# Kernel optimization log

Measured on AMD Instinct MI355X. Metric: run time of the kernel, lower is better.

The kernel has to match this reference:

```python
import jax, jax.numpy as jnp
import numpy as np

B, S, D, H = 4, 2048, 1024, 16
DK = D // H


def setup_inputs() -> dict:
    key = jax.random.key(0)
    ks = jax.random.split(key, 11)
    inp = {
        'query': jax.random.normal(ks[0], (B, S, D), jnp.float32),
        'key': jax.random.normal(ks[1], (B, S, D), jnp.float32),
        'value': jax.random.normal(ks[2], (B, S, D), jnp.float32),
        'mask': jnp.tril(jnp.ones((1, 1, S, S), dtype=bool)),  # causal
    }
    sc = 1.0 / np.sqrt(D)
    inp['w_q'] = jax.random.normal(ks[3], (D, D), jnp.float32) * sc
    inp['b_q'] = jnp.zeros((D,), jnp.float32)
    inp['w_k'] = jax.random.normal(ks[4], (D, D), jnp.float32) * sc
    inp['b_k'] = jnp.zeros((D,), jnp.float32)
    inp['w_v'] = jax.random.normal(ks[5], (D, D), jnp.float32) * sc
    inp['b_v'] = jnp.zeros((D,), jnp.float32)
    inp['w_o'] = jax.random.normal(ks[6], (D, D), jnp.float32) * sc
    inp['b_o'] = jnp.zeros((D,), jnp.float32)
    return inp


def _split_heads(x):
    # Faithful to source: view(B, S, d_k, H) then permute(0,3,1,2)
    b, s, _ = x.shape
    return x.reshape(b, s, DK, H).transpose(0, 3, 1, 2)  # (B, H, S, DK)


def _concat_heads(x):
    # permute(0,2,1,3) -> reshape(B, S, d_k*H)
    b, h, s, dk = x.shape
    return x.transpose(0, 2, 1, 3).reshape(b, s, dk * h)


def reference(query, key, value, mask, w_q, b_q, w_k, b_k, w_v, b_v, w_o, b_o):
    q = query @ w_q.T + b_q
    k = key @ w_k.T + b_k
    v = value @ w_v.T + b_v
    q, k, v = _split_heads(q), _split_heads(k), _split_heads(v)
    scale = 1.0 / jnp.sqrt(jnp.asarray(DK, q.dtype))
    scores = jnp.einsum('bhqd,bhkd->bhqk', q, k) * scale
    scores = jnp.where(mask, scores, -jnp.inf)
    attn = jax.nn.softmax(scores, axis=-1)  # dropout p=0 -> identity
    out = jnp.einsum('bhqk,bhkd->bhqd', attn, v)
    return _concat_heads(out) @ w_o.T + b_o
```

## Files before the change

kernel.cpp:

```cpp
#include <hip/hip_runtime.h>

#define BB 4
#define SS 2048
#define DD 1024
#define HH 16
#define DK 64
#define MM (BB * SS)

typedef __bf16 bf16x8 __attribute__((ext_vector_type(8)));
typedef float f32x4 __attribute__((ext_vector_type(4)));
typedef unsigned short us8 __attribute__((ext_vector_type(8)));
typedef unsigned short us4 __attribute__((ext_vector_type(4)));

#define MFMA_BF16(a, b, c) __builtin_amdgcn_mfma_f32_16x16x32_bf16((a), (b), (c), 0, 0, 0)

__device__ __forceinline__ unsigned short f2bf(float f) {
  return __builtin_bit_cast(unsigned short, (__bf16)f);
}

__device__ __forceinline__ bf16x8 ld_frag(const unsigned short* p) {
  return __builtin_bit_cast(bf16x8, *(const us8*)p);
}

__device__ __forceinline__ void gl_lds16(const unsigned short* g, unsigned short* l) {
  __builtin_amdgcn_global_load_lds((const __attribute__((address_space(1))) void*)g,
                                   (__attribute__((address_space(3))) void*)l, 16, 0, 0);
}

__global__ void cvt_weights(const float* __restrict__ w0, const float* __restrict__ w1,
                            const float* __restrict__ w2, const float* __restrict__ w3,
                            unsigned short* __restrict__ dst) {
  const float* src = (blockIdx.y == 0) ? w0 : (blockIdx.y == 1) ? w1 : (blockIdx.y == 2) ? w2 : w3;
  unsigned short* d = dst + (size_t)blockIdx.y * (DD * DD);
  int idx = (blockIdx.x * 256 + threadIdx.x) * 4;
  float4 v = *(const float4*)(src + idx);
  us4 o;
  o[0] = f2bf(v.x); o[1] = f2bf(v.y); o[2] = f2bf(v.z); o[3] = f2bf(v.w);
  *(us4*)(d + idx) = o;
}

__global__ void cvt_x(const float* __restrict__ src, unsigned short* __restrict__ dst) {
  int idx = (blockIdx.x * 256 + threadIdx.x) * 8;
  float4 v0 = *(const float4*)(src + idx);
  float4 v1 = *(const float4*)(src + idx + 4);
  us8 o;
  o[0] = f2bf(v0.x); o[1] = f2bf(v0.y); o[2] = f2bf(v0.z); o[3] = f2bf(v0.w);
  o[4] = f2bf(v1.x); o[5] = f2bf(v1.y); o[6] = f2bf(v1.z); o[7] = f2bf(v1.w);
  *(us8*)(dst + idx) = o;
}

template <bool VMODE>
__global__ __launch_bounds__(256, 4) void qkv_gemm(
    const unsigned short* __restrict__ xb, const unsigned short* __restrict__ w,
    const float* __restrict__ bias, unsigned short* __restrict__ outp) {
  const int m0 = blockIdx.x * 128;
  const int h0 = blockIdx.y * 2;

  __shared__ unsigned short smem[17408];
  unsigned short* sA = smem;
  unsigned short* sB = smem + 4096;

  const int tid = threadIdx.x;
  const int lane = tid & 63;
  const int wave = tid >> 6;
  const int wm = wave & 1, wn = wave >> 1;
  const int quad = lane >> 4, l16 = lane & 15;

  f32x4 acc[4][4];
#pragma unroll
  for (int i = 0; i < 4; i++)
#pragma unroll
    for (int j = 0; j < 4; j++) acc[i][j] = f32x4{0.f, 0.f, 0.f, 0.f};

  for (int k0 = 0; k0 < DD; k0 += 32) {
    __syncthreads();
#pragma unroll
    for (int i = 0; i < 2; i++) {
      int idx = tid + i * 256;
      gl_lds16(xb + (size_t)(m0 + (idx >> 2)) * DD + k0 + ((idx & 3) << 3), sA + idx * 8);
    }
#pragma unroll
    for (int i = 0; i < 2; i++) {
      int idx = tid + i * 256;
      int c = idx >> 2;
      int n = ((c & 63) << 4) + h0 + (c >> 6);
      gl_lds16(w + (size_t)n * DD + k0 + ((idx & 3) << 3), sB + idx * 8);
    }
    __syncthreads();
    bf16x8 af[4];
#pragma unroll
    for (int mi = 0; mi < 4; mi++)
      af[mi] = ld_frag(sA + (wm * 64 + mi * 16 + l16) * 32 + quad * 8);
#pragma unroll
    for (int ni = 0; ni < 4; ni++) {
      bf16x8 bfr = ld_frag(sB + (wn * 64 + ni * 16 + l16) * 32 + quad * 8);
#pragma unroll
      for (int mi = 0; mi < 4; mi++) acc[mi][ni] = MFMA_BF16(af[mi], bfr, acc[mi][ni]);
    }
  }

  if (!VMODE) {
#pragma unroll
    for (int mi = 0; mi < 4; mi++) {
#pragma unroll
      for (int ni = 0; ni < 4; ni++) {
        int c = wn * 64 + ni * 16 + l16;
        int h = h0 + (c >> 6), dk = c & 63;
        float bvv = bias[(dk << 4) + h];
        int mg0 = m0 + wm * 64 + mi * 16 + quad * 4;
#pragma unroll
        for (int r = 0; r < 4; r++) {
          int mg = mg0 + r;
          int bb = mg >> 11, s = mg & 2047;
          size_t dst = ((size_t)((bb << 4) + h) * SS + s) * DK + dk;
          outp[dst] = f2bf(acc[mi][ni][r] + bvv);
        }
      }
    }
  } else {
    __syncthreads();
#pragma unroll
    for (int mi = 0; mi < 4; mi++) {
#pragma unroll
      for (int ni = 0; ni < 4; ni++) {
        int c = wn * 64 + ni * 16 + l16;
        int h = h0 + (c >> 6), dk = c & 63;
        float bvv = bias[(dk << 4) + h];
        int ml0 = wm * 64 + mi * 16 + quad * 4;
#pragma unroll
        for (int r = 0; r < 4; r++)
          smem[c * 136 + ml0 + r] = f2bf(acc[mi][ni][r] + bvv);
      }
    }
    __syncthreads();
    int bb = m0 >> 11;
    int sbase = m0 & 2047;
#pragma unroll
    for (int i = 0; i < 8; i++) {
      int idx = tid + i * 256;
      int c = idx >> 4, mc = (idx & 15) << 3;
      int h = h0 + (c >> 6), dk = c & 63;
      size_t dst = ((size_t)((bb << 4) + h) * DK + dk) * SS + sbase + mc;
      *(us8*)(outp + dst) = *(const us8*)(smem + c * 136 + mc);
    }
  }
}

__global__ __launch_bounds__(256, 2) void attn(
    const unsigned short* __restrict__ qh, const unsigned short* __restrict__ kh,
    const unsigned short* __restrict__ vt, unsigned short* __restrict__ outc) {
  const int bx = blockIdx.x;
  const int bh = blockIdx.y;
  const int b = bh >> 4, h = bh & 15;
  const unsigned short* Qp = qh + (size_t)bh * SS * DK;
  const unsigned short* Kp = kh + (size_t)bh * SS * DK;
  const unsigned short* Vp = vt + (size_t)bh * DK * SS;

  __shared__ unsigned short sK[128 * 72];
  __shared__ unsigned short sV[64 * 136];
  __shared__ unsigned short sP[128 * 132];

  const int tid = threadIdx.x;
  const int lane = tid & 63;
  const int wave = tid >> 6;
  const int quad = lane >> 4, l16 = lane & 15;
  const int wq0 = wave * 32;

  const float sl = 0.125f * 1.44269504088896f;

  for (int pass = 0; pass < 2; pass++) {
    const int qt = pass ? (15 - bx) : bx;
    const int q0 = qt * 128;

    bf16x8 aq[2][2];
#pragma unroll
    for (int mi = 0; mi < 2; mi++)
#pragma unroll
      for (int kk = 0; kk < 2; kk++)
        aq[mi][kk] = ld_frag(Qp + (size_t)(q0 + wq0 + mi * 16 + l16) * DK + kk * 32 + quad * 8);

    f32x4 o_acc[2][4];
    float mrowL[2], lrowL[2];
#pragma unroll
    for (int mi = 0; mi < 2; mi++) {
#pragma unroll
      for (int ni = 0; ni < 4; ni++) o_acc[mi][ni] = f32x4{0.f, 0.f, 0.f, 0.f};
      mrowL[mi] = -1e30f;
      lrowL[mi] = 0.f;
    }

    auto do_tile = [&](int kt, bool diag) {
      const int k0 = kt * 128;
      __syncthreads();
#pragma unroll
      for (int i = 0; i < 4; i++) {
        int idx = tid + i * 256;
        int row = idx >> 3, c8 = (idx & 7) << 3;
        *(us8*)(sK + row * 72 + c8) = *(const us8*)(Kp + (size_t)(k0 + row) * DK + c8);
      }
#pragma unroll
      for (int i = 0; i < 4; i++) {
        int idx = tid + i * 256;
        int row = idx >> 4, cc = (idx & 15) << 3;
        *(us8*)(sV + row * 136 + cc) = *(const us8*)(Vp + (size_t)row * SS + k0 + cc);
      }
      __syncthreads();

      f32x4 sc[2][8];
#pragma unroll
      for (int mi = 0; mi < 2; mi++)
#pragma unroll
        for (int kti = 0; kti < 8; kti++) sc[mi][kti] = f32x4{0.f, 0.f, 0.f, 0.f};
#pragma unroll
      for (int kti = 0; kti < 8; kti++) {
#pragma unroll
        for (int kk = 0; kk < 2; kk++) {
          bf16x8 ak = ld_frag(sK + (kti * 16 + l16) * 72 + kk * 32 + quad * 8);
#pragma unroll
          for (int mi = 0; mi < 2; mi++) sc[mi][kti] = MFMA_BF16(ak, aq[mi][kk], sc[mi][kti]);
        }
      }

      if (diag) {
#pragma unroll
        for (int mi = 0; mi < 2; mi++) {
          int ql = wq0 + mi * 16 + l16;
#pragma unroll
          for (int kti = 0; kti < 8; kti++)
#pragma unroll
            for (int r = 0; r < 4; r++) {
              int kl = kti * 16 + quad * 4 + r;
              float v = sc[mi][kti][r] * sl;
              sc[mi][kti][r] = (kl > ql) ? -1e30f : v;
            }
        }
      } else {
#pragma unroll
        for (int mi = 0; mi < 2; mi++)
#pragma unroll
          for (int kti = 0; kti < 8; kti++)
#pragma unroll
            for (int r = 0; r < 4; r++) sc[mi][kti][r] *= sl;
      }

      float alphaL[2];
#pragma unroll
      for (int mi = 0; mi < 2; mi++) {
        f32x4 vm = sc[mi][0];
#pragma unroll
        for (int kti = 1; kti < 8; kti++)
#pragma unroll
          for (int r = 0; r < 4; r++) vm[r] = fmaxf(vm[r], sc[mi][kti][r]);
        float mx = fmaxf(fmaxf(vm[0], vm[1]), fmaxf(vm[2], vm[3]));
        mx = fmaxf(mx, __shfl_xor(mx, 16, 64));
        mx = fmaxf(mx, __shfl_xor(mx, 32, 64));
        float mnew = fmaxf(mrowL[mi], mx);
        alphaL[mi] = exp2f(mrowL[mi] - mnew);
        mrowL[mi] = mnew;
      }

#pragma unroll
      for (int mi = 0; mi < 2; mi++) {
        f32x4 vs = f32x4{0.f, 0.f, 0.f, 0.f};
#pragma unroll
        for (int kti = 0; kti < 8; kti++) {
          us4 pk;
#pragma unroll
          for (int r = 0; r < 4; r++) {
            float p = exp2f(sc[mi][kti][r] - mrowL[mi]);
            vs[r] += p;
            pk[r] = f2bf(p);
          }
          *(us4*)(sP + (wq0 + mi * 16 + l16) * 132 + kti * 16 + quad * 4) = pk;
        }
        float ls = (vs[0] + vs[1]) + (vs[2] + vs[3]);
        ls += __shfl_xor(ls, 16, 64);
        ls += __shfl_xor(ls, 32, 64);
        lrowL[mi] = lrowL[mi] * alphaL[mi] + ls;
      }

#pragma unroll
      for (int mi = 0; mi < 2; mi++)
#pragma unroll
        for (int r = 0; r < 4; r++) {
          float a = __shfl(alphaL[mi], quad * 4 + r, 64);
#pragma unroll
          for (int ni = 0; ni < 4; ni++) o_acc[mi][ni][r] *= a;
        }

#pragma unroll
      for (int kk = 0; kk < 4; kk++) {
        bf16x8 ap[2];
#pragma unroll
        for (int mi = 0; mi < 2; mi++) {
          const unsigned short* base = sP + (wq0 + mi * 16 + l16) * 132 + kk * 32 + quad * 8;
          us4 lo = *(const us4*)base;
          us4 hi = *(const us4*)(base + 4);
          ap[mi] = __builtin_bit_cast(bf16x8, __builtin_shufflevector(lo, hi, 0, 1, 2, 3, 4, 5, 6, 7));
        }
#pragma unroll
        for (int ni = 0; ni < 4; ni++) {
          bf16x8 bfr = ld_frag(sV + (ni * 16 + l16) * 136 + kk * 32 + quad * 8);
#pragma unroll
          for (int mi = 0; mi < 2; mi++) o_acc[mi][ni] = MFMA_BF16(ap[mi], bfr, o_acc[mi][ni]);
        }
      }
    };

    for (int kt = 0; kt < qt; kt++) do_tile(kt, false);
    do_tile(qt, true);

#pragma unroll
    for (int mi = 0; mi < 2; mi++) {
#pragma unroll
      for (int r = 0; r < 4; r++) {
        float lr = __shfl(lrowL[mi], quad * 4 + r, 64);
        float inv = 1.0f / lr;
        int qg = q0 + wq0 + mi * 16 + quad * 4 + r;
        size_t rowbase = ((size_t)(b * SS + qg)) * DD + h * DK;
#pragma unroll
        for (int ni = 0; ni < 4; ni++) {
          int dk = ni * 16 + l16;
          outc[rowbase + dk] = f2bf(o_acc[mi][ni][r] * inv);
        }
      }
    }
  }
}

__global__ __launch_bounds__(256, 4) void out_proj(
    const unsigned short* __restrict__ ac, const unsigned short* __restrict__ wo,
    const float* __restrict__ bias, float* __restrict__ out) {
  const int m0 = blockIdx.x * 128;
  const int n0 = blockIdx.y * 128;
  __shared__ unsigned short sA[128 * 32];
  __shared__ unsigned short sB[128 * 32];

  const int tid = threadIdx.x;
  const int lane = tid & 63;
  const int wave = tid >> 6;
  const int wm = wave & 1, wn = wave >> 1;
  const int quad = lane >> 4, l16 = lane & 15;

  f32x4 acc[4][4];
#pragma unroll
  for (int i = 0; i < 4; i++)
#pragma unroll
    for (int j = 0; j < 4; j++) acc[i][j] = f32x4{0.f, 0.f, 0.f, 0.f};

  for (int k0 = 0; k0 < DD; k0 += 32) {
    __syncthreads();
#pragma unroll
    for (int i = 0; i < 2; i++) {
      int idx = tid + i * 256;
      gl_lds16(ac + (size_t)(m0 + (idx >> 2)) * DD + k0 + ((idx & 3) << 3), sA + idx * 8);
    }
#pragma unroll
    for (int i = 0; i < 2; i++) {
      int idx = tid + i * 256;
      gl_lds16(wo + (size_t)(n0 + (idx >> 2)) * DD + k0 + ((idx & 3) << 3), sB + idx * 8);
    }
    __syncthreads();
    bf16x8 af[4];
#pragma unroll
    for (int mi = 0; mi < 4; mi++)
      af[mi] = ld_frag(sA + (wm * 64 + mi * 16 + l16) * 32 + quad * 8);
#pragma unroll
    for (int ni = 0; ni < 4; ni++) {
      bf16x8 bfr = ld_frag(sB + (wn * 64 + ni * 16 + l16) * 32 + quad * 8);
#pragma unroll
      for (int mi = 0; mi < 4; mi++) acc[mi][ni] = MFMA_BF16(af[mi], bfr, acc[mi][ni]);
    }
  }

#pragma unroll
  for (int mi = 0; mi < 4; mi++) {
#pragma unroll
    for (int ni = 0; ni < 4; ni++) {
      int n = n0 + wn * 64 + ni * 16 + l16;
      float bvv = bias[n];
      int mg0 = m0 + wm * 64 + mi * 16 + quad * 4;
#pragma unroll
      for (int r = 0; r < 4; r++) out[(size_t)(mg0 + r) * DD + n] = acc[mi][ni][r] + bvv;
    }
  }
}

extern "C" void kernel_launch(void* const* d_in, const int* in_sizes, int n_in,
                              void* d_out, int out_size, void* d_ws, size_t ws_size,
                              hipStream_t stream) {
  const float* q_in = (const float*)d_in[0];
  const float* k_in = (const float*)d_in[1];
  const float* v_in = (const float*)d_in[2];
  const float* w_q = (const float*)d_in[4];
  const float* b_q = (const float*)d_in[5];
  const float* w_k = (const float*)d_in[6];
  const float* b_k = (const float*)d_in[7];
  const float* w_v = (const float*)d_in[8];
  const float* b_v = (const float*)d_in[9];
  const float* w_o = (const float*)d_in[10];
  const float* b_o = (const float*)d_in[11];
  float* out = (float*)d_out;

  unsigned short* ws = (unsigned short*)d_ws;
  unsigned short* wb = ws;
  unsigned short* xb = ws + (size_t)4 * 1024 * 1024;
  unsigned short* qh = ws + (size_t)12 * 1024 * 1024;
  unsigned short* kh = ws + (size_t)20 * 1024 * 1024;
  unsigned short* vt = ws + (size_t)28 * 1024 * 1024;
  unsigned short* outc = xb;

  const size_t WSZ = (size_t)DD * DD;

  cvt_weights<<<dim3(1024, 4), 256, 0, stream>>>(w_q, w_k, w_v, w_o, wb);
  cvt_x<<<4096, 256, 0, stream>>>(q_in, xb);
  qkv_gemm<false><<<dim3(64, 8), 256, 0, stream>>>(xb, wb + 0 * WSZ, b_q, qh);
  cvt_x<<<4096, 256, 0, stream>>>(k_in, xb);
  qkv_gemm<false><<<dim3(64, 8), 256, 0, stream>>>(xb, wb + 1 * WSZ, b_k, kh);
  cvt_x<<<4096, 256, 0, stream>>>(v_in, xb);
  qkv_gemm<true><<<dim3(64, 8), 256, 0, stream>>>(xb, wb + 2 * WSZ, b_v, vt);
  attn<<<dim3(8, 64), 256, 0, stream>>>(qh, kh, vt, outc);
  out_proj<<<dim3(64, 8), 256, 0, stream>>>(outc, wb + 3 * WSZ, b_o, out);
}
```

Baseline: 384.9 us.

## Fuse input conversion into single QKV GEMM launch and retile attention to register-resident P

Drops the separate fp32-to-bf16 input conversion kernels: the QKV GEMM now loads fp32 activations, converts them in registers, and writes them to LDS. It also merges the three projections into one launch using blockIdx.z. The attention kernel moves to 64-row query tiles with one 16-row slice per wave, keeps P in registers instead of staging it through LDS, and raises occupancy. The output projection uses narrower N tiles to launch more blocks. The intent is to remove extra launches and memory round trips and to improve occupancy. In exchange the GEMMs reuse each loaded tile less and the attention kernel reloads K/V tiles more often.

```diff
diff --git a/kernel.cpp b/kernel.cpp
--- a/kernel.cpp
+++ b/kernel.cpp
@@ -39,24 +39,21 @@
   *(us4*)(d + idx) = o;
 }
 
-__global__ void cvt_x(const float* __restrict__ src, unsigned short* __restrict__ dst) {
-  int idx = (blockIdx.x * 256 + threadIdx.x) * 8;
-  float4 v0 = *(const float4*)(src + idx);
-  float4 v1 = *(const float4*)(src + idx + 4);
-  us8 o;
-  o[0] = f2bf(v0.x); o[1] = f2bf(v0.y); o[2] = f2bf(v0.z); o[3] = f2bf(v0.w);
-  o[4] = f2bf(v1.x); o[5] = f2bf(v1.y); o[6] = f2bf(v1.z); o[7] = f2bf(v1.w);
-  *(us8*)(dst + idx) = o;
-}
-
-template <bool VMODE>
 __global__ __launch_bounds__(256, 4) void qkv_gemm(
-    const unsigned short* __restrict__ xb, const unsigned short* __restrict__ w,
-    const float* __restrict__ bias, unsigned short* __restrict__ outp) {
+    const float* __restrict__ xq, const float* __restrict__ xk, const float* __restrict__ xv,
+    const unsigned short* __restrict__ wb,
+    const float* __restrict__ bq, const float* __restrict__ bk, const float* __restrict__ bv,
+    unsigned short* __restrict__ qh, unsigned short* __restrict__ kh,
+    unsigned short* __restrict__ vt) {
+  const int mode = blockIdx.z;
+  const float* x = (mode == 0) ? xq : (mode == 1) ? xk : xv;
+  const unsigned short* w = wb + (size_t)mode * (DD * DD);
+  const float* bias = (mode == 0) ? bq : (mode == 1) ? bk : bv;
+
   const int m0 = blockIdx.x * 128;
-  const int h0 = blockIdx.y * 2;
-
-  __shared__ unsigned short smem[17408];
+  const int h = blockIdx.y;
+
+  __shared__ unsigned short smem[8704];
   unsigned short* sA = smem;
   unsigned short* sB = smem + 4096;
 
@@ -66,25 +63,31 @@
   const int wm = wave & 1, wn = wave >> 1;
   const int quad = lane >> 4, l16 = lane & 15;
 
-  f32x4 acc[4][4];
+  f32x4 acc[4][2];
 #pragma unroll
   for (int i = 0; i < 4; i++)
 #pragma unroll
-    for (int j = 0; j < 4; j++) acc[i][j] = f32x4{0.f, 0.f, 0.f, 0.f};
+    for (int j = 0; j < 2; j++) acc[i][j] = f32x4{0.f, 0.f, 0.f, 0.f};
+
+  const int arow = tid >> 1, aoff = (tid & 1) << 4;
+  const float* ag = x + (size_t)(m0 + arow) * DD + aoff;
+  const unsigned short* bg = w + (size_t)(((tid >> 2) << 4) + h) * DD + ((tid & 3) << 3);
 
   for (int k0 = 0; k0 < DD; k0 += 32) {
     __syncthreads();
-#pragma unroll
-    for (int i = 0; i < 2; i++) {
-      int idx = tid + i * 256;
-      gl_lds16(xb + (size_t)(m0 + (idx >> 2)) * DD + k0 + ((idx & 3) << 3), sA + idx * 8);
-    }
-#pragma unroll
-    for (int i = 0; i < 2; i++) {
-      int idx = tid + i * 256;
-      int c = idx >> 2;
-      int n = ((c & 63) << 4) + h0 + (c >> 6);
-      gl_lds16(w + (size_t)n * DD + k0 + ((idx & 3) << 3), sB + idx * 8);
+    gl_lds16(bg + k0, sB + tid * 8);
+    {
+      float4 v0 = *(const float4*)(ag + k0);
+      float4 v1 = *(const float4*)(ag + k0 + 4);
+      float4 v2 = *(const float4*)(ag + k0 + 8);
+      float4 v3 = *(const float4*)(ag + k0 + 12);
+      us8 o0, o1;
+      o0[0] = f2bf(v0.x); o0[1] = f2bf(v0.y); o0[2] = f2bf(v0.z); o0[3] = f2bf(v0.w);
+      o0[4] = f2bf(v1.x); o0[5] = f2bf(v1.y); o0[6] = f2bf(v1.z); o0[7] = f2bf(v1.w);
+      o1[0] = f2bf(v2.x); o1[1] = f2bf(v2.y); o1[2] = f2bf(v2.z); o1[3] = f2bf(v2.w);
+      o1[4] = f2bf(v3.x); o1[5] = f2bf(v3.y); o1[6] = f2bf(v3.z); o1[7] = f2bf(v3.w);
+      *(us8*)(sA + arow * 32 + aoff) = o0;
+      *(us8*)(sA + arow * 32 + aoff + 8) = o1;
     }
     __syncthreads();
     bf16x8 af[4];
@@ -92,20 +95,20 @@
     for (int mi = 0; mi < 4; mi++)
       af[mi] = ld_frag(sA + (wm * 64 + mi * 16 + l16) * 32 + quad * 8);
 #pragma unroll
-    for (int ni = 0; ni < 4; ni++) {
-      bf16x8 bfr = ld_frag(sB + (wn * 64 + ni * 16 + l16) * 32 + quad * 8);
+    for (int ni = 0; ni < 2; ni++) {
+      bf16x8 bfr = ld_frag(sB + (wn * 32 + ni * 16 + l16) * 32 + quad * 8);
 #pragma unroll
       for (int mi = 0; mi < 4; mi++) acc[mi][ni] = MFMA_BF16(af[mi], bfr, acc[mi][ni]);
     }
   }
 
-  if (!VMODE) {
+  if (mode < 2) {
+    unsigned short* outp = (mode == 0) ? qh : kh;
 #pragma unroll
     for (int mi = 0; mi < 4; mi++) {
 #pragma unroll
-      for (int ni = 0; ni < 4; ni++) {
-        int c = wn * 64 + ni * 16 + l16;
-        int h = h0 + (c >> 6), dk = c & 63;
+      for (int ni = 0; ni < 2; ni++) {
+        int dk = wn * 32 + ni * 16 + l16;
         float bvv = bias[(dk << 4) + h];
         int mg0 = m0 + wm * 64 + mi * 16 + quad * 4;
 #pragma unroll
@@ -122,31 +125,29 @@
 #pragma unroll
     for (int mi = 0; mi < 4; mi++) {
 #pragma unroll
-      for (int ni = 0; ni < 4; ni++) {
-        int c = wn * 64 + ni * 16 + l16;
-        int h = h0 + (c >> 6), dk = c & 63;
+      for (int ni = 0; ni < 2; ni++) {
+        int dk = wn * 32 + ni * 16 + l16;
         float bvv = bias[(dk << 4) + h];
         int ml0 = wm * 64 + mi * 16 + quad * 4;
 #pragma unroll
         for (int r = 0; r < 4; r++)
-          smem[c * 136 + ml0 + r] = f2bf(acc[mi][ni][r] + bvv);
+          smem[dk * 136 + ml0 + r] = f2bf(acc[mi][ni][r] + bvv);
       }
     }
     __syncthreads();
     int bb = m0 >> 11;
     int sbase = m0 & 2047;
 #pragma unroll
-    for (int i = 0; i < 8; i++) {
+    for (int i = 0; i < 4; i++) {
       int idx = tid + i * 256;
-      int c = idx >> 4, mc = (idx & 15) << 3;
-      int h = h0 + (c >> 6), dk = c & 63;
+      int dk = idx >> 4, mc = (idx & 15) << 3;
       size_t dst = ((size_t)((bb << 4) + h) * DK + dk) * SS + sbase + mc;
-      *(us8*)(outp + dst) = *(const us8*)(smem + c * 136 + mc);
-    }
-  }
-}
-
-__global__ __launch_bounds__(256, 2) void attn(
+      *(us8*)(vt + dst) = *(const us8*)(smem + dk * 136 + mc);
+    }
+  }
+}
+
+__global__ __launch_bounds__(256, 4) void attn(
     const unsigned short* __restrict__ qh, const unsigned short* __restrict__ kh,
     const unsigned short* __restrict__ vt, unsigned short* __restrict__ outc) {
   const int bx = blockIdx.x;
@@ -158,39 +159,33 @@
 
   __shared__ unsigned short sK[128 * 72];
   __shared__ unsigned short sV[64 * 136];
-  __shared__ unsigned short sP[128 * 132];
 
   const int tid = threadIdx.x;
   const int lane = tid & 63;
   const int wave = tid >> 6;
   const int quad = lane >> 4, l16 = lane & 15;
-  const int wq0 = wave * 32;
 
   const float sl = 0.125f * 1.44269504088896f;
 
   for (int pass = 0; pass < 2; pass++) {
-    const int qt = pass ? (15 - bx) : bx;
-    const int q0 = qt * 128;
-
-    bf16x8 aq[2][2];
-#pragma unroll
-    for (int mi = 0; mi < 2; mi++)
-#pragma unroll
-      for (int kk = 0; kk < 2; kk++)
-        aq[mi][kk] = ld_frag(Qp + (size_t)(q0 + wq0 + mi * 16 + l16) * DK + kk * 32 + quad * 8);
-
-    f32x4 o_acc[2][4];
-    float mrowL[2], lrowL[2];
-#pragma unroll
-    for (int mi = 0; mi < 2; mi++) {
-#pragma unroll
-      for (int ni = 0; ni < 4; ni++) o_acc[mi][ni] = f32x4{0.f, 0.f, 0.f, 0.f};
-      mrowL[mi] = -1e30f;
-      lrowL[mi] = 0.f;
-    }
-
-    auto do_tile = [&](int kt, bool diag) {
+    const int qt = pass ? (31 - bx) : bx;
+    const int q0 = qt * 64;
+    const int qrow0 = q0 + wave * 16;
+    const int KT = (qt >> 1) + 1;
+
+    bf16x8 aq[2];
+#pragma unroll
+    for (int kk = 0; kk < 2; kk++)
+      aq[kk] = ld_frag(Qp + (size_t)(qrow0 + l16) * DK + kk * 32 + quad * 8);
+
+    f32x4 o_acc[4];
+    float mL = -1e30f, lL = 0.f;
+#pragma unroll
+    for (int ni = 0; ni < 4; ni++) o_acc[ni] = f32x4{0.f, 0.f, 0.f, 0.f};
+
+    for (int kt = 0; kt < KT; kt++) {
       const int k0 = kt * 128;
+      const bool last = (kt == KT - 1);
       __syncthreads();
 #pragma unroll
       for (int i = 0; i < 4; i++) {
@@ -206,125 +201,99 @@
       }
       __syncthreads();
 
-      f32x4 sc[2][8];
-#pragma unroll
-      for (int mi = 0; mi < 2; mi++)
-#pragma unroll
-        for (int kti = 0; kti < 8; kti++) sc[mi][kti] = f32x4{0.f, 0.f, 0.f, 0.f};
+      f32x4 sc[8];
+#pragma unroll
+      for (int kti = 0; kti < 8; kti++) sc[kti] = f32x4{0.f, 0.f, 0.f, 0.f};
 #pragma unroll
       for (int kti = 0; kti < 8; kti++) {
 #pragma unroll
         for (int kk = 0; kk < 2; kk++) {
           bf16x8 ak = ld_frag(sK + (kti * 16 + l16) * 72 + kk * 32 + quad * 8);
-#pragma unroll
-          for (int mi = 0; mi < 2; mi++) sc[mi][kti] = MFMA_BF16(ak, aq[mi][kk], sc[mi][kti]);
+          sc[kti] = MFMA_BF16(ak, aq[kk], sc[kti]);
         }
       }
 
-      if (diag) {
-#pragma unroll
-        for (int mi = 0; mi < 2; mi++) {
-          int ql = wq0 + mi * 16 + l16;
-#pragma unroll
-          for (int kti = 0; kti < 8; kti++)
-#pragma unroll
-            for (int r = 0; r < 4; r++) {
-              int kl = kti * 16 + quad * 4 + r;
-              float v = sc[mi][kti][r] * sl;
-              sc[mi][kti][r] = (kl > ql) ? -1e30f : v;
-            }
+      if (last) {
+        int qrel = qrow0 + l16 - k0;
+#pragma unroll
+        for (int kti = 0; kti < 8; kti++)
+#pragma unroll
+          for (int r = 0; r < 4; r++) {
+            int kl = kti * 16 + quad * 4 + r;
+            float v = sc[kti][r] * sl;
+            sc[kti][r] = (kl > qrel) ? -1e30f : v;
+          }
+      } else {
+#pragma unroll
+        for (int kti = 0; kti < 8; kti++)
+#pragma unroll
+          for (int r = 0; r < 4; r++) sc[kti][r] *= sl;
+      }
+
+      f32x4 vm = sc[0];
+#pragma unroll
+      for (int kti = 1; kti < 8; kti++)
+#pragma unroll
+        for (int r = 0; r < 4; r++) vm[r] = fmaxf(vm[r], sc[kti][r]);
+      float mx = fmaxf(fmaxf(vm[0], vm[1]), fmaxf(vm[2], vm[3]));
+      mx = fmaxf(mx, __shfl_xor(mx, 16, 64));
+      mx = fmaxf(mx, __shfl_xor(mx, 32, 64));
+      float mnew = fmaxf(mL, mx);
+      float alphaL = exp2f(mL - mnew);
+      mL = mnew;
+
+      us4 pk[8];
+      f32x4 vs = f32x4{0.f, 0.f, 0.f, 0.f};
+#pragma unroll
+      for (int kti = 0; kti < 8; kti++) {
+#pragma unroll
+        for (int r = 0; r < 4; r++) {
+          float p = exp2f(sc[kti][r] - mL);
+          vs[r] += p;
+          pk[kti][r] = f2bf(p);
         }
-      } else {
-#pragma unroll
-        for (int mi = 0; mi < 2; mi++)
-#pragma unroll
-          for (int kti = 0; kti < 8; kti++)
-#pragma unroll
-            for (int r = 0; r < 4; r++) sc[mi][kti][r] *= sl;
-      }
-
-      float alphaL[2];
-#pragma unroll
-      for (int mi = 0; mi < 2; mi++) {
-        f32x4 vm = sc[mi][0];
-#pragma unroll
-        for (int kti = 1; kti < 8; kti++)
-#pragma unroll
-          for (int r = 0; r < 4; r++) vm[r] = fmaxf(vm[r], sc[mi][kti][r]);
-        float mx = fmaxf(fmaxf(vm[0], vm[1]), fmaxf(vm[2], vm[3]));
-        mx = fmaxf(mx, __shfl_xor(mx, 16, 64));
-        mx = fmaxf(mx, __shfl_xor(mx, 32, 64));
-        float mnew = fmaxf(mrowL[mi], mx);
-        alphaL[mi] = exp2f(mrowL[mi] - mnew);
-        mrowL[mi] = mnew;
-      }
-
-#pragma unroll
-      for (int mi = 0; mi < 2; mi++) {
-        f32x4 vs = f32x4{0.f, 0.f, 0.f, 0.f};
-#pragma unroll
-        for (int kti = 0; kti < 8; kti++) {
-          us4 pk;
-#pragma unroll
-          for (int r = 0; r < 4; r++) {
-            float p = exp2f(sc[mi][kti][r] - mrowL[mi]);
-            vs[r] += p;
-            pk[r] = f2bf(p);
-          }
-          *(us4*)(sP + (wq0 + mi * 16 + l16) * 132 + kti * 16 + quad * 4) = pk;
+      }
+      float ls = (vs[0] + vs[1]) + (vs[2] + vs[3]);
+      ls += __shfl_xor(ls, 16, 64);
+      ls += __shfl_xor(ls, 32, 64);
+      lL = lL * alphaL + ls;
+
+#pragma unroll
+      for (int r = 0; r < 4; r++) {
+        float a = __shfl(alphaL, quad * 4 + r, 64);
+#pragma unroll
+        for (int ni = 0; ni < 4; ni++) o_acc[ni][r] *= a;
+      }
+
+#pragma unroll
+      for (int c = 0; c < 4; c++) {
+        bf16x8 ap = __builtin_bit_cast(
+            bf16x8, __builtin_shufflevector(pk[2 * c], pk[2 * c + 1], 0, 1, 2, 3, 4, 5, 6, 7));
+#pragma unroll
+        for (int ni = 0; ni < 4; ni++) {
+          const unsigned short* vb = sV + (ni * 16 + l16) * 136 + c * 32 + quad * 4;
+          us4 lo = *(const us4*)vb;
+          us4 hi = *(const us4*)(vb + 16);
+          bf16x8 bfr = __builtin_bit_cast(
+              bf16x8, __builtin_shufflevector(lo, hi, 0, 1, 2, 3, 4, 5, 6, 7));
+          o_acc[ni] = MFMA_BF16(ap, bfr, o_acc[ni]);
         }
-        float ls = (vs[0] + vs[1]) + (vs[2] + vs[3]);
-        ls += __shfl_xor(ls, 16, 64);
-        ls += __shfl_xor(ls, 32, 64);
-        lrowL[mi] = lrowL[mi] * alphaL[mi] + ls;
-      }
-
-#pragma unroll
-      for (int mi = 0; mi < 2; mi++)
-#pragma unroll
-        for (int r = 0; r < 4; r++) {
-          float a = __shfl(alphaL[mi], quad * 4 + r, 64);
-#pragma unroll
-          for (int ni = 0; ni < 4; ni++) o_acc[mi][ni][r] *= a;
-        }
-
-#pragma unroll
-      for (int kk = 0; kk < 4; kk++) {
-        bf16x8 ap[2];
-#pragma unroll
-        for (int mi = 0; mi < 2; mi++) {
-          const unsigned short* base = sP + (wq0 + mi * 16 + l16) * 132 + kk * 32 + quad * 8;
-          us4 lo = *(const us4*)base;
-          us4 hi = *(const us4*)(base + 4);
-          ap[mi] = __builtin_bit_cast(bf16x8, __builtin_shufflevector(lo, hi, 0, 1, 2, 3, 4, 5, 6, 7));
-        }
-#pragma unroll
-        for (int ni = 0; ni < 4; ni++) {
-          bf16x8 bfr = ld_frag(sV + (ni * 16 + l16) * 136 + kk * 32 + quad * 8);
-#pragma unroll
-          for (int mi = 0; mi < 2; mi++) o_acc[mi][ni] = MFMA_BF16(ap[mi], bfr, o_acc[mi][ni]);
-        }
-      }
-    };
-
-    for (int kt = 0; kt < qt; kt++) do_tile(kt, false);
-    do_tile(qt, true);
-
-#pragma unroll
-    for (int mi = 0; mi < 2; mi++) {
-#pragma unroll
-      for (int r = 0; r < 4; r++) {
-        float lr = __shfl(lrowL[mi], quad * 4 + r, 64);
-        float inv = 1.0f / lr;
-        int qg = q0 + wq0 + mi * 16 + quad * 4 + r;
-        size_t rowbase = ((size_t)(b * SS + qg)) * DD + h * DK;
-#pragma unroll
-        for (int ni = 0; ni < 4; ni++) {
-          int dk = ni * 16 + l16;
-          outc[rowbase + dk] = f2bf(o_acc[mi][ni][r] * inv);
-        }
-      }
-    }
+      }
+    }
+
+#pragma unroll
+    for (int r = 0; r < 4; r++) {
+      float lr = __shfl(lL, quad * 4 + r, 64);
+      float inv = 1.0f / lr;
+      int qg = qrow0 + quad * 4 + r;
+      size_t rowbase = ((size_t)(b * SS + qg)) * DD + h * DK;
+#pragma unroll
+      for (int ni = 0; ni < 4; ni++) {
+        int dk = ni * 16 + l16;
+        outc[rowbase + dk] = f2bf(o_acc[ni][r] * inv);
+      }
+    }
+    __syncthreads();
   }
 }
 
@@ -332,9 +301,9 @@
     const unsigned short* __restrict__ ac, const unsigned short* __restrict__ wo,
     const float* __restrict__ bias, float* __restrict__ out) {
   const int m0 = blockIdx.x * 128;
-  const int n0 = blockIdx.y * 128;
+  const int n0 = blockIdx.y * 64;
   __shared__ unsigned short sA[128 * 32];
-  __shared__ unsigned short sB[128 * 32];
+  __shared__ unsigned short sB[64 * 32];
 
   const int tid = threadIdx.x;
   const int lane = tid & 63;
@@ -342,32 +311,29 @@
   const int wm = wave & 1, wn = wave >> 1;
   const int quad = lane >> 4, l16 = lane & 15;
 
-  f32x4 acc[4][4];
+  f32x4 acc[4][2];
 #pragma unroll
   for (int i = 0; i < 4; i++)
 #pragma unroll
-    for (int j = 0; j < 4; j++) acc[i][j] = f32x4{0.f, 0.f, 0.f, 0.f};
+    for (int j = 0; j < 2; j++) acc[i][j] = f32x4{0.f, 0.f, 0.f, 0.f};
+
+  const unsigned short* ag = ac + (size_t)(m0 + (tid >> 2)) * DD + ((tid & 3) << 3);
+  const unsigned short* ag2 = ac + (size_t)(m0 + 64 + (tid >> 2)) * DD + ((tid & 3) << 3);
+  const unsigned short* bg = wo + (size_t)(n0 + (tid >> 2)) * DD + ((tid & 3) << 3);
 
   for (int k0 = 0; k0 < DD; k0 += 32) {
     __syncthreads();
-#pragma unroll
-    for (int i = 0; i < 2; i++) {
-      int idx = tid + i * 256;
-      gl_lds16(ac + (size_t)(m0 + (idx >> 2)) * DD + k0 + ((idx & 3) << 3), sA + idx * 8);
-    }
-#pragma unroll
-    for (int i = 0; i < 2; i++) {
-      int idx = tid + i * 256;
-      gl_lds16(wo + (size_t)(n0 + (idx >> 2)) * DD + k0 + ((idx & 3) << 3), sB + idx * 8);
-    }
+    gl_lds16(ag + k0, sA + tid * 8);
+    gl_lds16(ag2 + k0, sA + 2048 + tid * 8);
+    gl_lds16(bg + k0, sB + tid * 8);
     __syncthreads();
     bf16x8 af[4];
 #pragma unroll
     for (int mi = 0; mi < 4; mi++)
       af[mi] = ld_frag(sA + (wm * 64 + mi * 16 + l16) * 32 + quad * 8);
 #pragma unroll
-    for (int ni = 0; ni < 4; ni++) {
-      bf16x8 bfr = ld_frag(sB + (wn * 64 + ni * 16 + l16) * 32 + quad * 8);
+    for (int ni = 0; ni < 2; ni++) {
+      bf16x8 bfr = ld_frag(sB + (wn * 32 + ni * 16 + l16) * 32 + quad * 8);
 #pragma unroll
       for (int mi = 0; mi < 4; mi++) acc[mi][ni] = MFMA_BF16(af[mi], bfr, acc[mi][ni]);
     }
@@ -376,8 +342,8 @@
 #pragma unroll
   for (int mi = 0; mi < 4; mi++) {
 #pragma unroll
-    for (int ni = 0; ni < 4; ni++) {
-      int n = n0 + wn * 64 + ni * 16 + l16;
+    for (int ni = 0; ni < 2; ni++) {
+      int n = n0 + wn * 32 + ni * 16 + l16;
       float bvv = bias[n];
       int mg0 = m0 + wm * 64 + mi * 16 + quad * 4;
 #pragma unroll
@@ -404,21 +370,15 @@
 
   unsigned short* ws = (unsigned short*)d_ws;
   unsigned short* wb = ws;
-  unsigned short* xb = ws + (size_t)4 * 1024 * 1024;
-  unsigned short* qh = ws + (size_t)12 * 1024 * 1024;
-  unsigned short* kh = ws + (size_t)20 * 1024 * 1024;
-  unsigned short* vt = ws + (size_t)28 * 1024 * 1024;
-  unsigned short* outc = xb;
+  unsigned short* qh = ws + (size_t)4 * 1024 * 1024;
+  unsigned short* kh = ws + (size_t)12 * 1024 * 1024;
+  unsigned short* vt = ws + (size_t)20 * 1024 * 1024;
+  unsigned short* outc = ws + (size_t)28 * 1024 * 1024;
 
   const size_t WSZ = (size_t)DD * DD;
 
   cvt_weights<<<dim3(1024, 4), 256, 0, stream>>>(w_q, w_k, w_v, w_o, wb);
-  cvt_x<<<4096, 256, 0, stream>>>(q_in, xb);
-  qkv_gemm<false><<<dim3(64, 8), 256, 0, stream>>>(xb, wb + 0 * WSZ, b_q, qh);
-  cvt_x<<<4096, 256, 0, stream>>>(k_in, xb);
-  qkv_gemm<false><<<dim3(64, 8), 256, 0, stream>>>(xb, wb + 1 * WSZ, b_k, kh);
-  cvt_x<<<4096, 256, 0, stream>>>(v_in, xb);
-  qkv_gemm<true><<<dim3(64, 8), 256, 0, stream>>>(xb, wb + 2 * WSZ, b_v, vt);
-  attn<<<dim3(8, 64), 256, 0, stream>>>(qh, kh, vt, outc);
-  out_proj<<<dim3(64, 8), 256, 0, stream>>>(outc, wb + 3 * WSZ, b_o, out);
-}
+  qkv_gemm<<<dim3(64, 16, 3), 256, 0, stream>>>(q_in, k_in, v_in, wb, b_q, b_k, b_v, qh, kh, vt);
+  attn<<<dim3(16, 64), 256, 0, stream>>>(qh, kh, vt, outc);
+  out_proj<<<dim3(64, 16), 256, 0, stream>>>(outc, wb + 3 * WSZ, b_o, out);
+}
```

Result: slower. 409.7 us (+6.4%).

## Fuse input conversion into batched QKV GEMM and keep P in registers

Applied to the files above, without the earlier changes.

Drops the separate fp32-to-bf16 input conversion kernels. The QKV GEMM now loads fp32 activations directly, converts them in registers, and runs all three projections in one z-batched launch. The GEMM K-step is widened to 64 in both the QKV and output GEMMs. In attention, the P tile stays in registers instead of going through LDS, with the V fragment loads permuted to match; this frees LDS so the occupancy hint rises to 3 and the grid order is swapped. The risks are higher register pressure and that the A-side fp32 loads are synchronous, with no global-to-LDS async path.

```diff
diff --git a/kernel.cpp b/kernel.cpp
--- a/kernel.cpp
+++ b/kernel.cpp
@@ -39,26 +39,23 @@
   *(us4*)(d + idx) = o;
 }
 
-__global__ void cvt_x(const float* __restrict__ src, unsigned short* __restrict__ dst) {
-  int idx = (blockIdx.x * 256 + threadIdx.x) * 8;
-  float4 v0 = *(const float4*)(src + idx);
-  float4 v1 = *(const float4*)(src + idx + 4);
-  us8 o;
-  o[0] = f2bf(v0.x); o[1] = f2bf(v0.y); o[2] = f2bf(v0.z); o[3] = f2bf(v0.w);
-  o[4] = f2bf(v1.x); o[5] = f2bf(v1.y); o[6] = f2bf(v1.z); o[7] = f2bf(v1.w);
-  *(us8*)(dst + idx) = o;
-}
-
-template <bool VMODE>
 __global__ __launch_bounds__(256, 4) void qkv_gemm(
-    const unsigned short* __restrict__ xb, const unsigned short* __restrict__ w,
-    const float* __restrict__ bias, unsigned short* __restrict__ outp) {
+    const float* __restrict__ xq, const float* __restrict__ xk, const float* __restrict__ xv,
+    const unsigned short* __restrict__ wb,
+    const float* __restrict__ bq, const float* __restrict__ bk, const float* __restrict__ bv,
+    unsigned short* __restrict__ qh, unsigned short* __restrict__ kh,
+    unsigned short* __restrict__ vt) {
+  const int mode = blockIdx.z;
+  const float* x = (mode == 0) ? xq : (mode == 1) ? xk : xv;
+  const unsigned short* w = wb + (size_t)mode * (DD * DD);
+  const float* bias = (mode == 0) ? bq : (mode == 1) ? bk : bv;
+
   const int m0 = blockIdx.x * 128;
   const int h0 = blockIdx.y * 2;
 
   __shared__ unsigned short smem[17408];
   unsigned short* sA = smem;
-  unsigned short* sB = smem + 4096;
+  unsigned short* sB = smem + 8192;
 
   const int tid = threadIdx.x;
   const int lane = tid & 63;
@@ -72,34 +69,64 @@
 #pragma unroll
     for (int j = 0; j < 4; j++) acc[i][j] = f32x4{0.f, 0.f, 0.f, 0.f};
 
-  for (int k0 = 0; k0 < DD; k0 += 32) {
-    __syncthreads();
-#pragma unroll
-    for (int i = 0; i < 2; i++) {
-      int idx = tid + i * 256;
-      gl_lds16(xb + (size_t)(m0 + (idx >> 2)) * DD + k0 + ((idx & 3) << 3), sA + idx * 8);
-    }
-#pragma unroll
-    for (int i = 0; i < 2; i++) {
-      int idx = tid + i * 256;
-      int c = idx >> 2;
-      int n = ((c & 63) << 4) + h0 + (c >> 6);
-      gl_lds16(w + (size_t)n * DD + k0 + ((idx & 3) << 3), sB + idx * 8);
-    }
-    __syncthreads();
-    bf16x8 af[4];
-#pragma unroll
-    for (int mi = 0; mi < 4; mi++)
-      af[mi] = ld_frag(sA + (wm * 64 + mi * 16 + l16) * 32 + quad * 8);
-#pragma unroll
-    for (int ni = 0; ni < 4; ni++) {
-      bf16x8 bfr = ld_frag(sB + (wn * 64 + ni * 16 + l16) * 32 + quad * 8);
-#pragma unroll
-      for (int mi = 0; mi < 4; mi++) acc[mi][ni] = MFMA_BF16(af[mi], bfr, acc[mi][ni]);
+  const int arow = tid >> 1, ahalf = tid & 1;
+  const float* ag = x + (size_t)(m0 + arow) * DD + ahalf * 32;
+  unsigned short* adst = sA + ahalf * 4096 + arow * 32;
+
+  for (int k0 = 0; k0 < DD; k0 += 64) {
+    __syncthreads();
+#pragma unroll
+    for (int j = 0; j < 4; j++) {
+      int cid = tid + j * 256;
+      int half = cid >> 9;
+      int rr = (cid & 511) >> 2;
+      int c8 = (cid & 3) << 3;
+      int n = ((rr & 63) << 4) + h0 + (rr >> 6);
+      gl_lds16(w + (size_t)n * DD + k0 + half * 32 + c8,
+               sB + half * 4096 + rr * 32 + c8);
+    }
+    {
+      const float* a = ag + k0;
+      float4 v0 = *(const float4*)(a + 0);
+      float4 v1 = *(const float4*)(a + 4);
+      float4 v2 = *(const float4*)(a + 8);
+      float4 v3 = *(const float4*)(a + 12);
+      float4 v4 = *(const float4*)(a + 16);
+      float4 v5 = *(const float4*)(a + 20);
+      float4 v6 = *(const float4*)(a + 24);
+      float4 v7 = *(const float4*)(a + 28);
+      us8 o0, o1, o2, o3;
+      o0[0] = f2bf(v0.x); o0[1] = f2bf(v0.y); o0[2] = f2bf(v0.z); o0[3] = f2bf(v0.w);
+      o0[4] = f2bf(v1.x); o0[5] = f2bf(v1.y); o0[6] = f2bf(v1.z); o0[7] = f2bf(v1.w);
+      o1[0] = f2bf(v2.x); o1[1] = f2bf(v2.y); o1[2] = f2bf(v2.z); o1[3] = f2bf(v2.w);
+      o1[4] = f2bf(v3.x); o1[5] = f2bf(v3.y); o1[6] = f2bf(v3.z); o1[7] = f2bf(v3.w);
+      o2[0] = f2bf(v4.x); o2[1] = f2bf(v4.y); o2[2] = f2bf(v4.z); o2[3] = f2bf(v4.w);
+      o2[4] = f2bf(v5.x); o2[5] = f2bf(v5.y); o2[6] = f2bf(v5.z); o2[7] = f2bf(v5.w);
+      o3[0] = f2bf(v6.x); o3[1] = f2bf(v6.y); o3[2] = f2bf(v6.z); o3[3] = f2bf(v6.w);
+      o3[4] = f2bf(v7.x); o3[5] = f2bf(v7.y); o3[6] = f2bf(v7.z); o3[7] = f2bf(v7.w);
+      *(us8*)(adst + 0) = o0;
+      *(us8*)(adst + 8) = o1;
+      *(us8*)(adst + 16) = o2;
+      *(us8*)(adst + 24) = o3;
+    }
+    __syncthreads();
+#pragma unroll
+    for (int kk = 0; kk < 2; kk++) {
+      bf16x8 af[4];
+#pragma unroll
+      for (int mi = 0; mi < 4; mi++)
+        af[mi] = ld_frag(sA + kk * 4096 + (wm * 64 + mi * 16 + l16) * 32 + quad * 8);
+#pragma unroll
+      for (int ni = 0; ni < 4; ni++) {
+        bf16x8 bfr = ld_frag(sB + kk * 4096 + (wn * 64 + ni * 16 + l16) * 32 + quad * 8);
+#pragma unroll
+        for (int mi = 0; mi < 4; mi++) acc[mi][ni] = MFMA_BF16(af[mi], bfr, acc[mi][ni]);
+      }
     }
   }
 
-  if (!VMODE) {
+  if (mode < 2) {
+    unsigned short* outp = (mode == 0) ? qh : kh;
 #pragma unroll
     for (int mi = 0; mi < 4; mi++) {
 #pragma unroll
@@ -141,16 +168,16 @@
       int c = idx >> 4, mc = (idx & 15) << 3;
       int h = h0 + (c >> 6), dk = c & 63;
       size_t dst = ((size_t)((bb << 4) + h) * DK + dk) * SS + sbase + mc;
-      *(us8*)(outp + dst) = *(const us8*)(smem + c * 136 + mc);
+      *(us8*)(vt + dst) = *(const us8*)(smem + c * 136 + mc);
     }
   }
 }
 
-__global__ __launch_bounds__(256, 2) void attn(
+__global__ __launch_bounds__(256, 3) void attn(
     const unsigned short* __restrict__ qh, const unsigned short* __restrict__ kh,
     const unsigned short* __restrict__ vt, unsigned short* __restrict__ outc) {
-  const int bx = blockIdx.x;
-  const int bh = blockIdx.y;
+  const int bh = blockIdx.x;
+  const int by = blockIdx.y;
   const int b = bh >> 4, h = bh & 15;
   const unsigned short* Qp = qh + (size_t)bh * SS * DK;
   const unsigned short* Kp = kh + (size_t)bh * SS * DK;
@@ -158,7 +185,6 @@
 
   __shared__ unsigned short sK[128 * 72];
   __shared__ unsigned short sV[64 * 136];
-  __shared__ unsigned short sP[128 * 132];
 
   const int tid = threadIdx.x;
   const int lane = tid & 63;
@@ -169,7 +195,7 @@
   const float sl = 0.125f * 1.44269504088896f;
 
   for (int pass = 0; pass < 2; pass++) {
-    const int qt = pass ? (15 - bx) : bx;
+    const int qt = pass ? (15 - by) : by;
     const int q0 = qt * 128;
 
     bf16x8 aq[2][2];
@@ -189,8 +215,9 @@
       lrowL[mi] = 0.f;
     }
 
-    auto do_tile = [&](int kt, bool diag) {
+    for (int kt = 0; kt <= qt; kt++) {
       const int k0 = kt * 128;
+      const bool diag = (kt == qt);
       __syncthreads();
 #pragma unroll
       for (int i = 0; i < 4; i++) {
@@ -261,54 +288,44 @@
 
 #pragma unroll
       for (int mi = 0; mi < 2; mi++) {
+#pragma unroll
+        for (int r = 0; r < 4; r++) {
+          float a = __shfl(alphaL[mi], quad * 4 + r, 64);
+#pragma unroll
+          for (int ni = 0; ni < 4; ni++) o_acc[mi][ni][r] *= a;
+        }
+        us4 pk[8];
         f32x4 vs = f32x4{0.f, 0.f, 0.f, 0.f};
 #pragma unroll
         for (int kti = 0; kti < 8; kti++) {
-          us4 pk;
 #pragma unroll
           for (int r = 0; r < 4; r++) {
             float p = exp2f(sc[mi][kti][r] - mrowL[mi]);
             vs[r] += p;
-            pk[r] = f2bf(p);
+            pk[kti][r] = f2bf(p);
           }
-          *(us4*)(sP + (wq0 + mi * 16 + l16) * 132 + kti * 16 + quad * 4) = pk;
         }
         float ls = (vs[0] + vs[1]) + (vs[2] + vs[3]);
         ls += __shfl_xor(ls, 16, 64);
         ls += __shfl_xor(ls, 32, 64);
         lrowL[mi] = lrowL[mi] * alphaL[mi] + ls;
-      }
-
-#pragma unroll
-      for (int mi = 0; mi < 2; mi++)
-#pragma unroll
-        for (int r = 0; r < 4; r++) {
-          float a = __shfl(alphaL[mi], quad * 4 + r, 64);
-#pragma unroll
-          for (int ni = 0; ni < 4; ni++) o_acc[mi][ni][r] *= a;
-        }
-
-#pragma unroll
-      for (int kk = 0; kk < 4; kk++) {
-        bf16x8 ap[2];
-#pragma unroll
-        for (int mi = 0; mi < 2; mi++) {
-          const unsigned short* base = sP + (wq0 + mi * 16 + l16) * 132 + kk * 32 + quad * 8;
-          us4 lo = *(const us4*)base;
-          us4 hi = *(const us4*)(base + 4);
-          ap[mi] = __builtin_bit_cast(bf16x8, __builtin_shufflevector(lo, hi, 0, 1, 2, 3, 4, 5, 6, 7));
-        }
-#pragma unroll
-        for (int ni = 0; ni < 4; ni++) {
-          bf16x8 bfr = ld_frag(sV + (ni * 16 + l16) * 136 + kk * 32 + quad * 8);
-#pragma unroll
-          for (int mi = 0; mi < 2; mi++) o_acc[mi][ni] = MFMA_BF16(ap[mi], bfr, o_acc[mi][ni]);
-        }
-      }
-    };
-
-    for (int kt = 0; kt < qt; kt++) do_tile(kt, false);
-    do_tile(qt, true);
+
+#pragma unroll
+        for (int c = 0; c < 4; c++) {
+          bf16x8 ap = __builtin_bit_cast(
+              bf16x8, __builtin_shufflevector(pk[2 * c], pk[2 * c + 1], 0, 1, 2, 3, 4, 5, 6, 7));
+#pragma unroll
+          for (int ni = 0; ni < 4; ni++) {
+            const unsigned short* vb = sV + (ni * 16 + l16) * 136 + c * 32 + quad * 4;
+            us4 lo = *(const us4*)vb;
+            us4 hi = *(const us4*)(vb + 16);
+            bf16x8 bfr = __builtin_bit_cast(
+                bf16x8, __builtin_shufflevector(lo, hi, 0, 1, 2, 3, 4, 5, 6, 7));
+            o_acc[mi][ni] = MFMA_BF16(ap, bfr, o_acc[mi][ni]);
+          }
+        }
+      }
+    }
 
 #pragma unroll
     for (int mi = 0; mi < 2; mi++) {
@@ -325,6 +342,7 @@
         }
       }
     }
+    __syncthreads();
   }
 }
 
@@ -333,8 +351,8 @@
     const float* __restrict__ bias, float* __restrict__ out) {
   const int m0 = blockIdx.x * 128;
   const int n0 = blockIdx.y * 128;
-  __shared__ unsigned short sA[128 * 32];
-  __shared__ unsigned short sB[128 * 32];
+  __shared__ unsigned short sA[8192];
+  __shared__ unsigned short sB[8192];
 
   const int tid = threadIdx.x;
   const int lane = tid & 63;
@@ -348,28 +366,39 @@
 #pragma unroll
     for (int j = 0; j < 4; j++) acc[i][j] = f32x4{0.f, 0.f, 0.f, 0.f};
 
-  for (int k0 = 0; k0 < DD; k0 += 32) {
-    __syncthreads();
-#pragma unroll
-    for (int i = 0; i < 2; i++) {
-      int idx = tid + i * 256;
-      gl_lds16(ac + (size_t)(m0 + (idx >> 2)) * DD + k0 + ((idx & 3) << 3), sA + idx * 8);
-    }
-#pragma unroll
-    for (int i = 0; i < 2; i++) {
-      int idx = tid + i * 256;
-      gl_lds16(wo + (size_t)(n0 + (idx >> 2)) * DD + k0 + ((idx & 3) << 3), sB + idx * 8);
-    }
-    __syncthreads();
-    bf16x8 af[4];
-#pragma unroll
-    for (int mi = 0; mi < 4; mi++)
-      af[mi] = ld_frag(sA + (wm * 64 + mi * 16 + l16) * 32 + quad * 8);
-#pragma unroll
-    for (int ni = 0; ni < 4; ni++) {
-      bf16x8 bfr = ld_frag(sB + (wn * 64 + ni * 16 + l16) * 32 + quad * 8);
-#pragma unroll
-      for (int mi = 0; mi < 4; mi++) acc[mi][ni] = MFMA_BF16(af[mi], bfr, acc[mi][ni]);
+  for (int k0 = 0; k0 < DD; k0 += 64) {
+    __syncthreads();
+#pragma unroll
+    for (int j = 0; j < 4; j++) {
+      int cid = tid + j * 256;
+      int half = cid >> 9;
+      int rr = (cid & 511) >> 2;
+      int c8 = (cid & 3) << 3;
+      gl_lds16(ac + (size_t)(m0 + rr) * DD + k0 + half * 32 + c8,
+               sA + half * 4096 + rr * 32 + c8);
+    }
+#pragma unroll
+    for (int j = 0; j < 4; j++) {
+      int cid = tid + j * 256;
+      int half = cid >> 9;
+      int rr = (cid & 511) >> 2;
+      int c8 = (cid & 3) << 3;
+      gl_lds16(wo + (size_t)(n0 + rr) * DD + k0 + half * 32 + c8,
+               sB + half * 4096 + rr * 32 + c8);
+    }
+    __syncthreads();
+#pragma unroll
+    for (int kk = 0; kk < 2; kk++) {
+      bf16x8 af[4];
+#pragma unroll
+      for (int mi = 0; mi < 4; mi++)
+        af[mi] = ld_frag(sA + kk * 4096 + (wm * 64 + mi * 16 + l16) * 32 + quad * 8);
+#pragma unroll
+      for (int ni = 0; ni < 4; ni++) {
+        bf16x8 bfr = ld_frag(sB + kk * 4096 + (wn * 64 + ni * 16 + l16) * 32 + quad * 8);
+#pragma unroll
+        for (int mi = 0; mi < 4; mi++) acc[mi][ni] = MFMA_BF16(af[mi], bfr, acc[mi][ni]);
+      }
     }
   }
 
@@ -404,21 +433,15 @@
 
   unsigned short* ws = (unsigned short*)d_ws;
   unsigned short* wb = ws;
-  unsigned short* xb = ws + (size_t)4 * 1024 * 1024;
-  unsigned short* qh = ws + (size_t)12 * 1024 * 1024;
-  unsigned short* kh = ws + (size_t)20 * 1024 * 1024;
-  unsigned short* vt = ws + (size_t)28 * 1024 * 1024;
-  unsigned short* outc = xb;
+  unsigned short* qh = ws + (size_t)4 * 1024 * 1024;
+  unsigned short* kh = ws + (size_t)12 * 1024 * 1024;
+  unsigned short* vt = ws + (size_t)20 * 1024 * 1024;
+  unsigned short* outc = ws + (size_t)28 * 1024 * 1024;
 
   const size_t WSZ = (size_t)DD * DD;
 
   cvt_weights<<<dim3(1024, 4), 256, 0, stream>>>(w_q, w_k, w_v, w_o, wb);
-  cvt_x<<<4096, 256, 0, stream>>>(q_in, xb);
-  qkv_gemm<false><<<dim3(64, 8), 256, 0, stream>>>(xb, wb + 0 * WSZ, b_q, qh);
-  cvt_x<<<4096, 256, 0, stream>>>(k_in, xb);
-  qkv_gemm<false><<<dim3(64, 8), 256, 0, stream>>>(xb, wb + 1 * WSZ, b_k, kh);
-  cvt_x<<<4096, 256, 0, stream>>>(v_in, xb);
-  qkv_gemm<true><<<dim3(64, 8), 256, 0, stream>>>(xb, wb + 2 * WSZ, b_v, vt);
-  attn<<<dim3(8, 64), 256, 0, stream>>>(qh, kh, vt, outc);
+  qkv_gemm<<<dim3(64, 8, 3), 256, 0, stream>>>(q_in, k_in, v_in, wb, b_q, b_k, b_v, qh, kh, vt);
+  attn<<<dim3(64, 8), 256, 0, stream>>>(qh, kh, vt, outc);
   out_proj<<<dim3(64, 8), 256, 0, stream>>>(outc, wb + 3 * WSZ, b_o, out);
 }
```

Result: slower. 571.4 us (+48.4%).
